# Optimization experiments

Measured on AMD Instinct MI355X. Metric: run time of the kernel, lower is better.

## Reference

```python
import jax, jax.numpy as jnp
import numpy as np


def setup_inputs() -> dict:
    key = jax.random.key(0)
    k1, k2 = jax.random.split(key)
    num_tokens, top_k, num_experts = 1048576, 8, 64
    top_scores = jax.random.uniform(k1, (num_tokens, top_k), dtype=jnp.float32)
    selected_experts_indices = jax.random.randint(
        k2, (num_tokens, top_k), 0, num_experts, dtype=jnp.int64
    ) if jax.config.jax_enable_x64 else jax.random.randint(
        k2, (num_tokens, top_k), 0, num_experts, dtype=jnp.int32
    )
    return {
        "top_scores": top_scores,
        "selected_experts_indices": selected_experts_indices,
        "num_experts": num_experts,
    }


def reference(top_scores, selected_experts_indices, num_experts):
    flat_idx = selected_experts_indices.reshape(-1)  # [num_tokens*top_k]
    # histogram of tokens per expert (torch.histc returns float)
    num_tokens_per_expert = jnp.bincount(flat_idx, length=num_experts).astype(jnp.float32)
    # stable argsort by expert id -> permutation grouping tokens by expert
    token_indices_experts_sorted = jnp.argsort(flat_idx, stable=True)
    # gather routing scores into expert-sorted order
    top_scores_experts_sorted = top_scores.reshape(-1)[token_indices_experts_sorted]
    return (
        top_scores_experts_sorted,
        token_indices_experts_sorted,
        num_tokens_per_expert,
    )
```

## Files before the change

kernel.cpp:

```cpp
#include <hip/hip_runtime.h>


#define TILE 2048
#define WCH  512
#define RND  8

__device__ __forceinline__ unsigned long long match_mask(
    unsigned key,
    unsigned long long b0, unsigned long long b1, unsigned long long b2,
    unsigned long long b3, unsigned long long b4, unsigned long long b5,
    unsigned long long am) {
  unsigned long long m = am;
  m &= (key & 1u)  ? b0 : ~b0;
  m &= (key & 2u)  ? b1 : ~b1;
  m &= (key & 4u)  ? b2 : ~b2;
  m &= (key & 8u)  ? b3 : ~b3;
  m &= (key & 16u) ? b4 : ~b4;
  m &= (key & 32u) ? b5 : ~b5;
  return m;
}

__global__ __launch_bounds__(256) void hist_kernel(
    const int* __restrict__ idx, unsigned* __restrict__ countsT,
    int N, int nb) {
  __shared__ unsigned h[4][64];
  int wave = threadIdx.x >> 6;
  int lane = threadIdx.x & 63;
  h[wave][lane] = 0;
  __syncthreads();

  long long base = (long long)blockIdx.x * TILE;
  long long rem = (long long)N - base;
  if (rem >= TILE) {
    const int4* v = (const int4*)(idx + base);
    #pragma unroll
    for (int k = 0; k < TILE / 1024; ++k) {
      int4 x = v[threadIdx.x + k * 256];
      atomicAdd(&h[wave][((unsigned)x.x) & 63u], 1u);
      atomicAdd(&h[wave][((unsigned)x.y) & 63u], 1u);
      atomicAdd(&h[wave][((unsigned)x.z) & 63u], 1u);
      atomicAdd(&h[wave][((unsigned)x.w) & 63u], 1u);
    }
  } else if (rem > 0) {
    for (int j = threadIdx.x; j < (int)rem; j += 256)
      atomicAdd(&h[wave][((unsigned)idx[base + j]) & 63u], 1u);
  }
  __syncthreads();
  if (threadIdx.x < 64) {
    countsT[(size_t)threadIdx.x * nb + blockIdx.x] =
        h[0][threadIdx.x] + h[1][threadIdx.x] + h[2][threadIdx.x] + h[3][threadIdx.x];
  }
}

__global__ __launch_bounds__(256) void scan_kernel(
    unsigned* __restrict__ countsT, unsigned* __restrict__ totals,
    float* __restrict__ out_counts, int nb) {
  int e = blockIdx.x;
  int t = threadIdx.x;
  unsigned* row = countsT + (size_t)e * nb;
  int per = (nb + 255) >> 8;
  int base = t * per;

  unsigned s = 0;
  for (int j = 0; j < per; ++j) {
    int w = base + j;
    if (w < nb) s += row[w];
  }
  __shared__ unsigned sh[256];
  sh[t] = s;
  __syncthreads();
  for (int d = 1; d < 256; d <<= 1) {
    unsigned v = sh[t];
    unsigned a = (t >= d) ? sh[t - d] : 0u;
    __syncthreads();
    sh[t] = v + a;
    __syncthreads();
  }
  unsigned incl = sh[t];
  unsigned run = incl - s;
  for (int j = 0; j < per; ++j) {
    int w = base + j;
    if (w < nb) { unsigned v = row[w]; row[w] = run; run += v; }
  }
  if (t == 255) {
    totals[e] = incl;
    out_counts[e] = (float)incl;
  }
}

__global__ __launch_bounds__(256, 8) void scatter_kernel(
    const int* __restrict__ idx, const float* __restrict__ scores,
    const unsigned* __restrict__ baseT, const unsigned* __restrict__ totals,
    float* __restrict__ out_scores, float* __restrict__ out_idx,
    int N, int nb) {
  __shared__ uint2    sdat[TILE];
  __shared__ unsigned tmpc[4][64];
  __shared__ unsigned shc[4][64];
  __shared__ unsigned table[4][64];

  const int wave = threadIdx.x >> 6;
  const int lane = threadIdx.x & 63;
  const unsigned long long lt = (1ull << lane) - 1ull;

  const long long start = (long long)blockIdx.x * TILE + (long long)wave * WCH;
  const bool fullt = ((long long)(blockIdx.x + 1) * TILE) <= (long long)N;

  const unsigned tot = totals[lane];
  const unsigned gb0 = baseT[(size_t)lane * nb + blockIdx.x];

  unsigned e_pk[2] = {0, 0};
  unsigned r_pk[2] = {0, 0};
  unsigned c_pk[2] = {0, 0};
  unsigned wtotal = 0;

  if (fullt) {
    #pragma unroll
    for (int r = 0; r < RND; ++r) {
      long long i = start + r * 64 + lane;
      unsigned e = ((unsigned)idx[i]) & 63u;
      unsigned long long b0 = __ballot(e & 1u);
      unsigned long long b1 = __ballot(e & 2u);
      unsigned long long b2 = __ballot(e & 4u);
      unsigned long long b3 = __ballot(e & 8u);
      unsigned long long b4 = __ballot(e & 16u);
      unsigned long long b5 = __ballot(e & 32u);
      unsigned long long ms = match_mask(e, b0, b1, b2, b3, b4, b5, ~0ull);
      unsigned rank = (unsigned)__popcll(ms & lt);
      unsigned rcnt = (unsigned)__popcll(ms);
      tmpc[wave][lane] = 0;
      tmpc[wave][e] = rcnt;
      unsigned cnt = tmpc[wave][lane];
      const int q = r >> 2, sh = (r & 3) * 8;
      e_pk[q] |= e << sh;
      r_pk[q] |= rank << sh;
      c_pk[q] |= cnt << sh;
      wtotal += cnt;
    }
  } else {
    for (int j = threadIdx.x; j < TILE; j += 256) sdat[j].y = 0xFFFFFFFFu;
    __syncthreads();
    for (int r = 0; r < RND; ++r) {
      long long i = start + (long long)r * 64 + lane;
      bool valid = i < (long long)N;
      unsigned long long am = __ballot(valid ? 1 : 0);
      unsigned e = valid ? (((unsigned)idx[i]) & 63u) : 0u;
      unsigned long long b0 = __ballot(e & 1u);
      unsigned long long b1 = __ballot(e & 2u);
      unsigned long long b2 = __ballot(e & 4u);
      unsigned long long b3 = __ballot(e & 8u);
      unsigned long long b4 = __ballot(e & 16u);
      unsigned long long b5 = __ballot(e & 32u);
      unsigned long long ms = match_mask(e, b0, b1, b2, b3, b4, b5, am);
      unsigned rank = (unsigned)__popcll(ms & lt);
      unsigned rcnt = (unsigned)__popcll(ms);
      tmpc[wave][lane] = 0;
      if (valid) tmpc[wave][e] = rcnt;
      unsigned cnt = tmpc[wave][lane];
      const int q = r >> 2, sh = (r & 3) * 8;
      e_pk[q] |= e << sh;
      r_pk[q] |= rank << sh;
      c_pk[q] |= cnt << sh;
      wtotal += cnt;
    }
  }

  shc[wave][lane] = wtotal;

  unsigned sum = wtotal;
  #pragma unroll
  for (int d = 1; d < 64; d <<= 1) {
    unsigned nv = __shfl_up(sum, d, 64);
    if (lane >= d) sum += nv;
  }
  const unsigned ws_l = (unsigned)(wave * WCH) + (sum - wtotal);

  unsigned cur[RND];
  {
    unsigned acc = ws_l;
    #pragma unroll
    for (int r = 0; r < RND; ++r) {
      cur[r] = acc;
      acc += (c_pk[r >> 2] >> ((r & 3) * 8)) & 0xffu;
    }
  }

  __syncthreads();

  {
    unsigned s2 = tot;
    #pragma unroll
    for (int d = 1; d < 64; d <<= 1) {
      unsigned nv = __shfl_up(s2, d, 64);
      if (lane >= d) s2 += nv;
    }
    unsigned estart = s2 - tot;
    unsigned wpre = 0;
    for (int w2 = 0; w2 < wave; ++w2) wpre += shc[w2][lane];
    table[wave][lane] = estart + gb0 + wpre - ws_l;
  }

  if (fullt) {
    #pragma unroll
    for (int r = 0; r < RND; ++r) {
      long long i = start + r * 64 + lane;
      float s = scores[i];
      const int q = r >> 2, sh = (r & 3) * 8;
      unsigned e    = (e_pk[q] >> sh) & 0xffu;
      unsigned rank = (r_pk[q] >> sh) & 0xffu;
      unsigned pos = (unsigned)__shfl((int)cur[r], (int)e, 64) + rank;
      sdat[pos] = make_uint2(__float_as_uint(s), (((unsigned)i) << 6) | e);
    }
  } else {
    for (int r = 0; r < RND; ++r) {
      long long i = start + (long long)r * 64 + lane;
      bool valid = i < (long long)N;
      float s = valid ? scores[i] : 0.0f;
      const int q = r >> 2, sh = (r & 3) * 8;
      unsigned e    = (e_pk[q] >> sh) & 0xffu;
      unsigned rank = (r_pk[q] >> sh) & 0xffu;
      unsigned pos = (unsigned)__shfl((int)cur[r], (int)e, 64) + rank;
      if (valid) {
        sdat[pos] = make_uint2(__float_as_uint(s), (((unsigned)i) << 6) | e);
      }
    }
  }
  __syncthreads();

  if (fullt) {
    #pragma unroll
    for (int k = 0; k < TILE / 256; ++k) {
      int j = threadIdx.x + k * 256;
      uint2 v = sdat[j];
      unsigned e = v.y & 63u;
      int w = j >> 9;
      unsigned d = table[w][e] + (unsigned)j;
      out_scores[d] = __uint_as_float(v.x);
      out_idx[d] = (float)(v.y >> 6);
    }
  } else {
    for (int j = threadIdx.x; j < TILE; j += 256) {
      uint2 v = sdat[j];
      if (v.y == 0xFFFFFFFFu) continue;
      unsigned e = v.y & 63u;
      int w = j >> 9;
      unsigned d = table[w][e] + (unsigned)j;
      out_scores[d] = __uint_as_float(v.x);
      out_idx[d] = (float)(v.y >> 6);
    }
  }
}

extern "C" void kernel_launch(void* const* d_in, const int* in_sizes, int n_in,
                              void* d_out, int out_size, void* d_ws, size_t ws_size,
                              hipStream_t stream) {
  const float* scores = (const float*)d_in[0];
  const int* idx = (const int*)d_in[1];
  int N = in_sizes[0];

  float* out_scores = (float*)d_out;
  float* out_idx = out_scores + N;
  float* out_counts = out_idx + N;

  int nb = (N + TILE - 1) / TILE;
  unsigned* countsT = (unsigned*)d_ws;
  unsigned* totals = countsT + (size_t)64 * nb;

  hist_kernel<<<nb, 256, 0, stream>>>(idx, countsT, N, nb);
  scan_kernel<<<64, 256, 0, stream>>>(countsT, totals, out_counts, nb);
  scatter_kernel<<<nb, 256, 0, stream>>>(idx, scores, countsT, totals,
                                         out_scores, out_idx, N, nb);
}
```

Measured before the change: 144.9 us.

## Use ballot-based histograms, block-major counts layout, and block-wide local sort

Replaces the LDS-atomic histogram with wave ballot match masks, so each lane counts its own expert without atomics. Stores per-block counts block-major, which makes the histogram and scatter accesses coalesced, though the scan kernel now reads with a 64-element stride. The scatter kernel computes a block-wide expert ordering in shared memory so each expert's run within a block is contiguous, gives every expert a single destination offset, and loads scores early into registers. The cost is more ballot and ALU work per element and an extra block barrier.

```diff
diff --git a/kernel.cpp b/kernel.cpp
--- a/kernel.cpp
+++ b/kernel.cpp
@@ -24,30 +24,56 @@
     const int* __restrict__ idx, unsigned* __restrict__ countsT,
     int N, int nb) {
   __shared__ unsigned h[4][64];
-  int wave = threadIdx.x >> 6;
-  int lane = threadIdx.x & 63;
-  h[wave][lane] = 0;
-  __syncthreads();
+  const int wave = threadIdx.x >> 6;
+  const int lane = threadIdx.x & 63;
 
   long long base = (long long)blockIdx.x * TILE;
   long long rem = (long long)N - base;
+  unsigned cnt = 0;
+
   if (rem >= TILE) {
     const int4* v = (const int4*)(idx + base);
-    #pragma unroll
-    for (int k = 0; k < TILE / 1024; ++k) {
-      int4 x = v[threadIdx.x + k * 256];
-      atomicAdd(&h[wave][((unsigned)x.x) & 63u], 1u);
-      atomicAdd(&h[wave][((unsigned)x.y) & 63u], 1u);
-      atomicAdd(&h[wave][((unsigned)x.z) & 63u], 1u);
-      atomicAdd(&h[wave][((unsigned)x.w) & 63u], 1u);
-    }
-  } else if (rem > 0) {
-    for (int j = threadIdx.x; j < (int)rem; j += 256)
-      atomicAdd(&h[wave][((unsigned)idx[base + j]) & 63u], 1u);
-  }
+    int4 x0 = v[threadIdx.x];
+    int4 x1 = v[threadIdx.x + 256];
+    unsigned es[8] = {
+        ((unsigned)x0.x) & 63u, ((unsigned)x0.y) & 63u,
+        ((unsigned)x0.z) & 63u, ((unsigned)x0.w) & 63u,
+        ((unsigned)x1.x) & 63u, ((unsigned)x1.y) & 63u,
+        ((unsigned)x1.z) & 63u, ((unsigned)x1.w) & 63u};
+    #pragma unroll
+    for (int r = 0; r < 8; ++r) {
+      unsigned e = es[r];
+      unsigned long long b0 = __ballot(e & 1u);
+      unsigned long long b1 = __ballot(e & 2u);
+      unsigned long long b2 = __ballot(e & 4u);
+      unsigned long long b3 = __ballot(e & 8u);
+      unsigned long long b4 = __ballot(e & 16u);
+      unsigned long long b5 = __ballot(e & 32u);
+      cnt += (unsigned)__popcll(
+          match_mask((unsigned)lane, b0, b1, b2, b3, b4, b5, ~0ull));
+    }
+  } else {
+    long long wstart = base + (long long)wave * WCH;
+    for (int r = 0; r < RND; ++r) {
+      long long i = wstart + (long long)r * 64 + lane;
+      bool valid = i < (long long)N;
+      unsigned long long am = __ballot(valid ? 1 : 0);
+      unsigned e = valid ? (((unsigned)idx[i]) & 63u) : 0u;
+      unsigned long long b0 = __ballot(e & 1u);
+      unsigned long long b1 = __ballot(e & 2u);
+      unsigned long long b2 = __ballot(e & 4u);
+      unsigned long long b3 = __ballot(e & 8u);
+      unsigned long long b4 = __ballot(e & 16u);
+      unsigned long long b5 = __ballot(e & 32u);
+      cnt += (unsigned)__popcll(
+          match_mask((unsigned)lane, b0, b1, b2, b3, b4, b5, am));
+    }
+  }
+
+  h[wave][lane] = cnt;
   __syncthreads();
   if (threadIdx.x < 64) {
-    countsT[(size_t)threadIdx.x * nb + blockIdx.x] =
+    countsT[(size_t)blockIdx.x * 64 + threadIdx.x] =
         h[0][threadIdx.x] + h[1][threadIdx.x] + h[2][threadIdx.x] + h[3][threadIdx.x];
   }
 }
@@ -57,14 +83,13 @@
     float* __restrict__ out_counts, int nb) {
   int e = blockIdx.x;
   int t = threadIdx.x;
-  unsigned* row = countsT + (size_t)e * nb;
   int per = (nb + 255) >> 8;
   int base = t * per;
 
   unsigned s = 0;
   for (int j = 0; j < per; ++j) {
     int w = base + j;
-    if (w < nb) s += row[w];
+    if (w < nb) s += countsT[(size_t)w * 64 + e];
   }
   __shared__ unsigned sh[256];
   sh[t] = s;
@@ -80,7 +105,11 @@
   unsigned run = incl - s;
   for (int j = 0; j < per; ++j) {
     int w = base + j;
-    if (w < nb) { unsigned v = row[w]; row[w] = run; run += v; }
+    if (w < nb) {
+      unsigned v = countsT[(size_t)w * 64 + e];
+      countsT[(size_t)w * 64 + e] = run;
+      run += v;
+    }
   }
   if (t == 255) {
     totals[e] = incl;
@@ -94,9 +123,8 @@
     float* __restrict__ out_scores, float* __restrict__ out_idx,
     int N, int nb) {
   __shared__ uint2    sdat[TILE];
-  __shared__ unsigned tmpc[4][64];
   __shared__ unsigned shc[4][64];
-  __shared__ unsigned table[4][64];
+  __shared__ unsigned gdest[64];
 
   const int wave = threadIdx.x >> 6;
   const int lane = threadIdx.x & 63;
@@ -106,11 +134,12 @@
   const bool fullt = ((long long)(blockIdx.x + 1) * TILE) <= (long long)N;
 
   const unsigned tot = totals[lane];
-  const unsigned gb0 = baseT[(size_t)lane * nb + blockIdx.x];
+  const unsigned gb0 = baseT[(size_t)blockIdx.x * 64 + lane];
 
   unsigned e_pk[2] = {0, 0};
   unsigned r_pk[2] = {0, 0};
   unsigned c_pk[2] = {0, 0};
+  float    sreg[RND];
   unsigned wtotal = 0;
 
   if (fullt) {
@@ -118,6 +147,7 @@
     for (int r = 0; r < RND; ++r) {
       long long i = start + r * 64 + lane;
       unsigned e = ((unsigned)idx[i]) & 63u;
+      sreg[r] = scores[i];
       unsigned long long b0 = __ballot(e & 1u);
       unsigned long long b1 = __ballot(e & 2u);
       unsigned long long b2 = __ballot(e & 4u);
@@ -126,10 +156,8 @@
       unsigned long long b5 = __ballot(e & 32u);
       unsigned long long ms = match_mask(e, b0, b1, b2, b3, b4, b5, ~0ull);
       unsigned rank = (unsigned)__popcll(ms & lt);
-      unsigned rcnt = (unsigned)__popcll(ms);
-      tmpc[wave][lane] = 0;
-      tmpc[wave][e] = rcnt;
-      unsigned cnt = tmpc[wave][lane];
+      unsigned cnt  = (unsigned)__popcll(
+          match_mask((unsigned)lane, b0, b1, b2, b3, b4, b5, ~0ull));
       const int q = r >> 2, sh = (r & 3) * 8;
       e_pk[q] |= e << sh;
       r_pk[q] |= rank << sh;
@@ -144,6 +172,7 @@
       bool valid = i < (long long)N;
       unsigned long long am = __ballot(valid ? 1 : 0);
       unsigned e = valid ? (((unsigned)idx[i]) & 63u) : 0u;
+      sreg[r] = valid ? scores[i] : 0.0f;
       unsigned long long b0 = __ballot(e & 1u);
       unsigned long long b1 = __ballot(e & 2u);
       unsigned long long b2 = __ballot(e & 4u);
@@ -152,10 +181,8 @@
       unsigned long long b5 = __ballot(e & 32u);
       unsigned long long ms = match_mask(e, b0, b1, b2, b3, b4, b5, am);
       unsigned rank = (unsigned)__popcll(ms & lt);
-      unsigned rcnt = (unsigned)__popcll(ms);
-      tmpc[wave][lane] = 0;
-      if (valid) tmpc[wave][e] = rcnt;
-      unsigned cnt = tmpc[wave][lane];
+      unsigned cnt  = (unsigned)__popcll(
+          match_mask((unsigned)lane, b0, b1, b2, b3, b4, b5, am));
       const int q = r >> 2, sh = (r & 3) * 8;
       e_pk[q] |= e << sh;
       r_pk[q] |= rank << sh;
@@ -165,18 +192,28 @@
   }
 
   shc[wave][lane] = wtotal;
-
-  unsigned sum = wtotal;
+  __syncthreads();
+
+  unsigned c0 = shc[0][lane], c1 = shc[1][lane];
+  unsigned c2 = shc[2][lane], c3 = shc[3][lane];
+  unsigned bt = c0 + c1 + c2 + c3;
+  unsigned wpre = 0;
+  if (wave > 0) wpre += c0;
+  if (wave > 1) wpre += c1;
+  if (wave > 2) wpre += c2;
+
+  unsigned s = bt;
   #pragma unroll
   for (int d = 1; d < 64; d <<= 1) {
-    unsigned nv = __shfl_up(sum, d, 64);
-    if (lane >= d) sum += nv;
-  }
-  const unsigned ws_l = (unsigned)(wave * WCH) + (sum - wtotal);
+    unsigned nv = __shfl_up(s, d, 64);
+    if (lane >= d) s += nv;
+  }
+  unsigned bstart = s - bt;
+  unsigned wbase = bstart + wpre;
 
   unsigned cur[RND];
   {
-    unsigned acc = ws_l;
+    unsigned acc = wbase;
     #pragma unroll
     for (int r = 0; r < RND; ++r) {
       cur[r] = acc;
@@ -184,9 +221,7 @@
     }
   }
 
-  __syncthreads();
-
-  {
+  if (wave == 0) {
     unsigned s2 = tot;
     #pragma unroll
     for (int d = 1; d < 64; d <<= 1) {
@@ -194,33 +229,29 @@
       if (lane >= d) s2 += nv;
     }
     unsigned estart = s2 - tot;
-    unsigned wpre = 0;
-    for (int w2 = 0; w2 < wave; ++w2) wpre += shc[w2][lane];
-    table[wave][lane] = estart + gb0 + wpre - ws_l;
+    gdest[lane] = estart + gb0 - bstart;
   }
 
   if (fullt) {
     #pragma unroll
     for (int r = 0; r < RND; ++r) {
-      long long i = start + r * 64 + lane;
-      float s = scores[i];
+      unsigned i32 = (unsigned)(start + r * 64 + lane);
       const int q = r >> 2, sh = (r & 3) * 8;
       unsigned e    = (e_pk[q] >> sh) & 0xffu;
       unsigned rank = (r_pk[q] >> sh) & 0xffu;
       unsigned pos = (unsigned)__shfl((int)cur[r], (int)e, 64) + rank;
-      sdat[pos] = make_uint2(__float_as_uint(s), (((unsigned)i) << 6) | e);
+      sdat[pos] = make_uint2(__float_as_uint(sreg[r]), (i32 << 6) | e);
     }
   } else {
     for (int r = 0; r < RND; ++r) {
       long long i = start + (long long)r * 64 + lane;
       bool valid = i < (long long)N;
-      float s = valid ? scores[i] : 0.0f;
       const int q = r >> 2, sh = (r & 3) * 8;
       unsigned e    = (e_pk[q] >> sh) & 0xffu;
       unsigned rank = (r_pk[q] >> sh) & 0xffu;
       unsigned pos = (unsigned)__shfl((int)cur[r], (int)e, 64) + rank;
       if (valid) {
-        sdat[pos] = make_uint2(__float_as_uint(s), (((unsigned)i) << 6) | e);
+        sdat[pos] = make_uint2(__float_as_uint(sreg[r]), (((unsigned)i) << 6) | e);
       }
     }
   }
@@ -232,8 +263,7 @@
       int j = threadIdx.x + k * 256;
       uint2 v = sdat[j];
       unsigned e = v.y & 63u;
-      int w = j >> 9;
-      unsigned d = table[w][e] + (unsigned)j;
+      unsigned d = gdest[e] + (unsigned)j;
       out_scores[d] = __uint_as_float(v.x);
       out_idx[d] = (float)(v.y >> 6);
     }
@@ -242,8 +272,7 @@
       uint2 v = sdat[j];
       if (v.y == 0xFFFFFFFFu) continue;
       unsigned e = v.y & 63u;
-      int w = j >> 9;
-      unsigned d = table[w][e] + (unsigned)j;
+      unsigned d = gdest[e] + (unsigned)j;
       out_scores[d] = __uint_as_float(v.x);
       out_idx[d] = (float)(v.y >> 6);
     }
@@ -263,7 +292,7 @@
 
   int nb = (N + TILE - 1) / TILE;
   unsigned* countsT = (unsigned*)d_ws;
-  unsigned* totals = countsT + (size_t)64 * nb;
+  unsigned* totals = countsT + (size_t)nb * 64;
 
   hist_kernel<<<nb, 256, 0, stream>>>(idx, countsT, N, nb);
   scan_kernel<<<64, 256, 0, stream>>>(countsT, totals, out_counts, nb);
```

After: 151.8 us. 4.8% more time.
